# Performance work log

Hardware: AMD Instinct MI355X
Metric: run time of the kernel (lower is better)

## Reference

```python
import jax, jax.numpy as jnp
import numpy as np

N = 50000
E = 640000
F_IN = 128
F_OUT = 128


def setup_inputs() -> dict:
    key = jax.random.key(0)
    k1, k2, k3, k4, k5 = jax.random.split(key, 5)
    x = jax.random.normal(k1, (N, F_IN), dtype=jnp.float32)
    edge_index = jax.random.randint(k2, (2, E), 0, N, dtype=jnp.int64)
    s = 1.0 / np.sqrt(F_IN)
    W_l = jax.random.uniform(k3, (F_IN, F_OUT), minval=-s, maxval=s, dtype=jnp.float32)
    W_r = jax.random.uniform(k4, (F_IN, F_OUT), minval=-s, maxval=s, dtype=jnp.float32)
    b = jax.random.uniform(k5, (F_OUT,), minval=-s, maxval=s, dtype=jnp.float32)
    return {"x": x, "edge_index": edge_index, "W_l": W_l, "W_r": W_r, "b": b}


def reference(x, edge_index, W_l, W_r, b):
    src, dst = edge_index[0], edge_index[1]
    # gather source-node features along edges: [E, F_in]
    msgs = x[src]
    # mean aggregation at destination nodes
    summed = jax.ops.segment_sum(msgs, dst, num_segments=N)          # [N, F_in]
    counts = jax.ops.segment_sum(jnp.ones((E,), jnp.float32), dst, num_segments=N)
    mean_nb = summed / jnp.maximum(counts, 1.0)[:, None]
    # SAGEConv: lin_l(aggregated) + lin_r(self), bias on lin_l only
    out = mean_nb @ W_l + x @ W_r + b
    return jax.nn.relu(out)
```

## Files before the change

kernel.cpp:

```cpp
#include <hip/hip_runtime.h>

#define N_NODES 50000
#define E_EDGES 640000
#define F 128

typedef __attribute__((ext_vector_type(8))) short short8;
typedef __attribute__((ext_vector_type(4))) float f32x4;

#define DEG_OFF 0
#define OFF_OFF 200704
#define CUR_OFF 401408
#define BSUM_OFF 601600
#define BPRE_OFF 602624
#define WF_OFF 603648
#define SRC_OFF 734720
#define XBF_OFF 3294720
#define WS_NEED_FULL 16094720ULL

#define XCAST_BLKS 3125
#define WPREP_BLKS 16
#define HIST_BLKS 2048
#define PREP_GRID (XCAST_BLKS + WPREP_BLKS + HIST_BLKS)

__device__ __forceinline__ unsigned short f2bf(float f) {
    unsigned int u = __builtin_bit_cast(unsigned int, f);
    u += 0x7FFFu + ((u >> 16) & 1u);
    return (unsigned short)(u >> 16);
}
__device__ __forceinline__ float bfhi2f(unsigned int hi16) {
    return __builtin_bit_cast(float, hi16 & 0xFFFF0000u);
}

__global__ __launch_bounds__(256) void gnn_prep(
    const float* __restrict__ x, const int* __restrict__ ei,
    const float* __restrict__ Wl, const float* __restrict__ Wr,
    short* __restrict__ Wf, unsigned short* __restrict__ xbf,
    int* __restrict__ deg, int full) {
    const int bid = blockIdx.x;
    const int t = threadIdx.x;
    if (bid < XCAST_BLKS) {
        if (!full) return;
        const size_t i = ((size_t)bid * 256 + t) * 8;
        const float4 a0 = *reinterpret_cast<const float4*>(x + i);
        const float4 a1 = *reinterpret_cast<const float4*>(x + i + 4);
        short8 v;
        v[0] = (short)f2bf(a0.x); v[1] = (short)f2bf(a0.y);
        v[2] = (short)f2bf(a0.z); v[3] = (short)f2bf(a0.w);
        v[4] = (short)f2bf(a1.x); v[5] = (short)f2bf(a1.y);
        v[6] = (short)f2bf(a1.z); v[7] = (short)f2bf(a1.w);
        *reinterpret_cast<short8*>((short*)xbf + i) = v;
    } else if (bid < XCAST_BLKS + WPREP_BLKS) {
        const int tid = (bid - XCAST_BLKS) * 256 + t;
        const int lane = tid & 63;
        const int frag = tid >> 6;
        const int kstep = frag >> 3;
        const int ct = frag & 7;
        const int kb = kstep * 32 + (lane >> 4) * 8;
        const int c = ct * 16 + (lane & 15);
        short8 v;
#pragma unroll
        for (int j = 0; j < 8; ++j) {
            const int k = kb + j;
            const float f = (k < F) ? Wl[k * F + c] : Wr[(k - F) * F + c];
            v[j] = (short)f2bf(f);
        }
        *reinterpret_cast<short8*>(Wf + (size_t)tid * 8) = v;
    } else {
        const int i = (bid - XCAST_BLKS - WPREP_BLKS) * 256 + t;
        const int stride = HIST_BLKS * 256;
        for (int e = i; e < E_EDGES; e += stride)
            atomicAdd(&deg[ei[E_EDGES + e]], 1);
    }
}

__global__ __launch_bounds__(256) void gnn_scan_a(const int* __restrict__ deg,
                                                  int* __restrict__ off,
                                                  int* __restrict__ bsum) {
    __shared__ int s[256];
    const int t = threadIdx.x;
    const int i = blockIdx.x * 256 + t;
    const int v = (i < N_NODES) ? deg[i] : 0;
    s[t] = v;
    __syncthreads();
    for (int d = 1; d < 256; d <<= 1) {
        const int u = (t >= d) ? s[t - d] : 0;
        __syncthreads();
        s[t] += u;
        __syncthreads();
    }
    if (i < N_NODES) off[i] = s[t] - v;
    if (t == 255) bsum[blockIdx.x] = s[255];
}

__global__ __launch_bounds__(256) void gnn_scan2(const int* __restrict__ bsum,
                                                 int* __restrict__ off,
                                                 int* __restrict__ cur) {
    __shared__ int s[256];
    const int t = threadIdx.x;
    const int bid = blockIdx.x;
    s[t] = (t < 196) ? bsum[t] : 0;
    __syncthreads();
    for (int d = 1; d < 256; d <<= 1) {
        const int u = (t >= d) ? s[t - d] : 0;
        __syncthreads();
        s[t] += u;
        __syncthreads();
    }
    const int myPre = (bid == 0) ? 0 : s[bid - 1];
    const int i = bid * 256 + t;
    if (i < N_NODES) {
        const int o = off[i] + myPre;
        off[i] = o;
        cur[i] = o;
    }
    if (bid == 0 && t == 0) off[N_NODES] = s[195];
}

__global__ __launch_bounds__(256) void gnn_fill(const int* __restrict__ ei,
                                                int* __restrict__ cur,
                                                int* __restrict__ srcs) {
    const int i = blockIdx.x * blockDim.x + threadIdx.x;
    const int stride = gridDim.x * blockDim.x;
    for (int e = i; e < E_EDGES; e += stride) {
        const int d = ei[E_EDGES + e];
        const int p = atomicAdd(&cur[d], 1);
        srcs[p] = ei[e];
    }
}

__global__ __launch_bounds__(256) void gnn_agg_fin(
    const unsigned short* __restrict__ xbf, const int* __restrict__ off,
    const int* __restrict__ srcs, const short* __restrict__ Wf,
    const float* __restrict__ bias, float* __restrict__ out) {
    __shared__ unsigned short mean_s[64 * 128];
    const int t = threadIdx.x;
    const int lane = t & 63;
    const int wv = t >> 6;
    const int nb0 = blockIdx.x * 64;
    const int half = lane >> 5;
    const int l32 = lane & 31;

    for (int i = 0; i < 16; ++i) {
        const int node = nb0 + wv * 16 + i;
        if (node >= N_NODES) break;
        const int o0 = off[node];
        const int o1 = off[node + 1];
        const unsigned short* xb = xbf + (size_t)l32 * 4;
        f32x4 acc0 = {0.f, 0.f, 0.f, 0.f}, acc1 = {0.f, 0.f, 0.f, 0.f};
        f32x4 acc2 = {0.f, 0.f, 0.f, 0.f}, acc3 = {0.f, 0.f, 0.f, 0.f};
        int j = o0;
        for (; j + 8 <= o1; j += 8) {
            const uint2 a = *reinterpret_cast<const uint2*>(xb + (size_t)srcs[j + half] * F);
            const uint2 b = *reinterpret_cast<const uint2*>(xb + (size_t)srcs[j + 2 + half] * F);
            const uint2 c = *reinterpret_cast<const uint2*>(xb + (size_t)srcs[j + 4 + half] * F);
            const uint2 d = *reinterpret_cast<const uint2*>(xb + (size_t)srcs[j + 6 + half] * F);
            acc0[0] += bfhi2f(a.x << 16); acc0[1] += bfhi2f(a.x);
            acc0[2] += bfhi2f(a.y << 16); acc0[3] += bfhi2f(a.y);
            acc1[0] += bfhi2f(b.x << 16); acc1[1] += bfhi2f(b.x);
            acc1[2] += bfhi2f(b.y << 16); acc1[3] += bfhi2f(b.y);
            acc2[0] += bfhi2f(c.x << 16); acc2[1] += bfhi2f(c.x);
            acc2[2] += bfhi2f(c.y << 16); acc2[3] += bfhi2f(c.y);
            acc3[0] += bfhi2f(d.x << 16); acc3[1] += bfhi2f(d.x);
            acc3[2] += bfhi2f(d.y << 16); acc3[3] += bfhi2f(d.y);
        }
        for (; j + 4 <= o1; j += 4) {
            const uint2 a = *reinterpret_cast<const uint2*>(xb + (size_t)srcs[j + half] * F);
            const uint2 b = *reinterpret_cast<const uint2*>(xb + (size_t)srcs[j + 2 + half] * F);
            acc0[0] += bfhi2f(a.x << 16); acc0[1] += bfhi2f(a.x);
            acc0[2] += bfhi2f(a.y << 16); acc0[3] += bfhi2f(a.y);
            acc1[0] += bfhi2f(b.x << 16); acc1[1] += bfhi2f(b.x);
            acc1[2] += bfhi2f(b.y << 16); acc1[3] += bfhi2f(b.y);
        }
        for (; j < o1; j += 2) {
            const int jj = j + half;
            const uint2 a = *reinterpret_cast<const uint2*>(
                xb + (size_t)srcs[(jj < o1) ? jj : o0] * F);
            if (jj < o1) {
                acc0[0] += bfhi2f(a.x << 16); acc0[1] += bfhi2f(a.x);
                acc0[2] += bfhi2f(a.y << 16); acc0[3] += bfhi2f(a.y);
            }
        }
        acc0 += acc1 + acc2 + acc3;
        f32x4 o;
        o[0] = __shfl_xor(acc0[0], 32, 64);
        o[1] = __shfl_xor(acc0[1], 32, 64);
        o[2] = __shfl_xor(acc0[2], 32, 64);
        o[3] = __shfl_xor(acc0[3], 32, 64);
        acc0 += o;
        if (half == 0) {
            const float inv = 1.0f / (float)max(o1 - o0, 1);
            acc0 *= inv;
            ushort4 m;
            m.x = f2bf(acc0[0]); m.y = f2bf(acc0[1]);
            m.z = f2bf(acc0[2]); m.w = f2bf(acc0[3]);
            const int r = wv * 16 + i;
            const int byteoff = r * 256 + ((l32 * 8) ^ ((r & 7) << 4));
            *reinterpret_cast<ushort4*>((char*)mean_s + byteoff) = m;
        }
    }
    __syncthreads();

    const int rl = lane & 15;
    const int kg = lane >> 4;
    const int r0 = nb0 + wv * 16;
    const int arow = r0 + rl;
    const int arow_c = (arow < N_NODES) ? arow : (N_NODES - 1);
    const int rr = arow_c - nb0;

    f32x4 acc[8];
#pragma unroll
    for (int ct = 0; ct < 8; ++ct) acc[ct] = (f32x4){0.f, 0.f, 0.f, 0.f};

#pragma unroll
    for (int kstep = 0; kstep < 8; ++kstep) {
        short8 af;
        if (kstep < 4) {
            const int cb = (kstep * 64 + kg * 16) ^ ((rr & 7) << 4);
            af = *reinterpret_cast<const short8*>((const char*)mean_s +
                                                  rr * 256 + cb);
        } else {
            const int k0 = kstep * 32 + kg * 8 - F;
            af = *reinterpret_cast<const short8*>(xbf + (size_t)arow_c * F + k0);
        }
#pragma unroll
        for (int ct = 0; ct < 8; ++ct) {
            const short8 bf = *reinterpret_cast<const short8*>(
                Wf + (size_t)((kstep * 8 + ct) * 64 + lane) * 8);
            acc[ct] = __builtin_amdgcn_mfma_f32_16x16x32_bf16(af, bf, acc[ct],
                                                              0, 0, 0);
        }
    }

#pragma unroll
    for (int ct = 0; ct < 8; ++ct) {
        const int c = ct * 16 + rl;
        const float bv = bias[c];
#pragma unroll
        for (int r = 0; r < 4; ++r) {
            const int row = r0 + kg * 4 + r;
            if (row < N_NODES)
                out[(size_t)row * F + c] = fmaxf(acc[ct][r] + bv, 0.0f);
        }
    }
}

__global__ __launch_bounds__(256) void gnn_aggregate(
    const float* __restrict__ x, const int* __restrict__ off,
    const int* __restrict__ srcs, float* __restrict__ out) {
    const int node = blockIdx.x * 4 + (threadIdx.x >> 6);
    if (node >= N_NODES) return;
    const int lane = threadIdx.x & 63;
    const int half = lane >> 5;
    const int l32 = lane & 31;
    const int o0 = off[node];
    const int o1 = off[node + 1];
    f32x4 acc0 = {0.f, 0.f, 0.f, 0.f};
    f32x4 acc1 = {0.f, 0.f, 0.f, 0.f};
    int j = o0;
    for (; j + 4 <= o1; j += 4) {
        const int sA = srcs[j + half];
        const int sB = srcs[j + 2 + half];
        acc0 += *reinterpret_cast<const f32x4*>(x + (size_t)sA * F + l32 * 4);
        acc1 += *reinterpret_cast<const f32x4*>(x + (size_t)sB * F + l32 * 4);
    }
    for (; j < o1; j += 2) {
        const int jj = j + half;
        const int s = srcs[(jj < o1) ? jj : o0];
        f32x4 v = *reinterpret_cast<const f32x4*>(x + (size_t)s * F + l32 * 4);
        if (jj >= o1) v = (f32x4){0.f, 0.f, 0.f, 0.f};
        acc0 += v;
    }
    acc0 += acc1;
    f32x4 o;
    o[0] = __shfl_xor(acc0[0], 32, 64);
    o[1] = __shfl_xor(acc0[1], 32, 64);
    o[2] = __shfl_xor(acc0[2], 32, 64);
    o[3] = __shfl_xor(acc0[3], 32, 64);
    acc0 += o;
    if (half == 0) {
        const float inv = 1.0f / (float)max(o1 - o0, 1);
        acc0 *= inv;
        *reinterpret_cast<f32x4*>(out + (size_t)node * F + l32 * 4) = acc0;
    }
}

__global__ __launch_bounds__(256) void gnn_finalize_mfma(
    const float* __restrict__ x, const short* __restrict__ Wf,
    const float* __restrict__ bias, float* __restrict__ out) {
    const int t = threadIdx.x;
    const int lane = t & 63;
    const int wv = t >> 6;
    const int r0 = blockIdx.x * 64 + wv * 16;
    const int rl = lane & 15;
    const int kg = lane >> 4;
    const int arow = r0 + rl;
    const int arow_c = (arow < N_NODES) ? arow : (N_NODES - 1);
    f32x4 acc[8];
#pragma unroll
    for (int ct = 0; ct < 8; ++ct) acc[ct] = (f32x4){0.f, 0.f, 0.f, 0.f};
#pragma unroll
    for (int kstep = 0; kstep < 8; ++kstep) {
        const int k0 = kstep * 32 + kg * 8;
        const float* asrc = (kstep < 4) ? (out + (size_t)arow_c * F + k0)
                                        : (x + (size_t)arow_c * F + (k0 - F));
        const float4 a0 = *reinterpret_cast<const float4*>(asrc);
        const float4 a1 = *reinterpret_cast<const float4*>(asrc + 4);
        short8 af;
        af[0] = (short)f2bf(a0.x); af[1] = (short)f2bf(a0.y);
        af[2] = (short)f2bf(a0.z); af[3] = (short)f2bf(a0.w);
        af[4] = (short)f2bf(a1.x); af[5] = (short)f2bf(a1.y);
        af[6] = (short)f2bf(a1.z); af[7] = (short)f2bf(a1.w);
#pragma unroll
        for (int ct = 0; ct < 8; ++ct) {
            const short8 bf = *reinterpret_cast<const short8*>(
                Wf + (size_t)((kstep * 8 + ct) * 64 + lane) * 8);
            acc[ct] = __builtin_amdgcn_mfma_f32_16x16x32_bf16(af, bf, acc[ct],
                                                              0, 0, 0);
        }
    }
#pragma unroll
    for (int ct = 0; ct < 8; ++ct) {
        const int c = ct * 16 + rl;
        const float bv = bias[c];
#pragma unroll
        for (int r = 0; r < 4; ++r) {
            const int row = r0 + kg * 4 + r;
            if (row < N_NODES)
                out[(size_t)row * F + c] = fmaxf(acc[ct][r] + bv, 0.0f);
        }
    }
}

extern "C" void kernel_launch(void* const* d_in, const int* in_sizes, int n_in,
                              void* d_out, int out_size, void* d_ws,
                              size_t ws_size, hipStream_t stream) {
    const float* x = (const float*)d_in[0];
    const int* ei = (const int*)d_in[1];
    const float* Wl = (const float*)d_in[2];
    const float* Wr = (const float*)d_in[3];
    const float* b = (const float*)d_in[4];
    float* out = (float*)d_out;

    char* ws = (char*)d_ws;
    int* deg = (int*)(ws + DEG_OFF);
    int* off = (int*)(ws + OFF_OFF);
    int* cur = (int*)(ws + CUR_OFF);
    int* bsum = (int*)(ws + BSUM_OFF);
    short* Wf = (short*)(ws + WF_OFF);
    int* srcs = (int*)(ws + SRC_OFF);
    unsigned short* xbf = (unsigned short*)(ws + XBF_OFF);

    const int full = (ws_size >= WS_NEED_FULL) ? 1 : 0;

    hipMemsetAsync(deg, 0, N_NODES * sizeof(int), stream);
    gnn_prep<<<PREP_GRID, 256, 0, stream>>>(x, ei, Wl, Wr, Wf, xbf, deg, full);
    gnn_scan_a<<<196, 256, 0, stream>>>(deg, off, bsum);
    gnn_scan2<<<196, 256, 0, stream>>>(bsum, off, cur);
    gnn_fill<<<2048, 256, 0, stream>>>(ei, cur, srcs);

    if (full) {
        gnn_agg_fin<<<(N_NODES + 63) / 64, 256, 0, stream>>>(xbf, off, srcs,
                                                             Wf, b, out);
    } else {
        gnn_aggregate<<<(N_NODES + 3) / 4, 256, 0, stream>>>(x, off, srcs, out);
        gnn_finalize_mfma<<<(N_NODES + 63) / 64, 256, 0, stream>>>(x, Wf, b,
                                                                   out);
    }
}
```

Before: 207.2 us.

## Split fused aggregate+GEMM kernel into separate bf16 aggregate and finalize kernels

```diff
diff --git a/kernel.cpp b/kernel.cpp
--- a/kernel.cpp
+++ b/kernel.cpp
@@ -11,11 +11,11 @@
 #define OFF_OFF 200704
 #define CUR_OFF 401408
 #define BSUM_OFF 601600
-#define BPRE_OFF 602624
 #define WF_OFF 603648
 #define SRC_OFF 734720
 #define XBF_OFF 3294720
-#define WS_NEED_FULL 16094720ULL
+#define MBF_OFF 16094720
+#define WS_NEED_FULL 28894720ULL
 
 #define XCAST_BLKS 3125
 #define WPREP_BLKS 16
@@ -128,84 +128,80 @@
     }
 }
 
-__global__ __launch_bounds__(256) void gnn_agg_fin(
+__global__ __launch_bounds__(256) void gnn_aggregate_bf(
     const unsigned short* __restrict__ xbf, const int* __restrict__ off,
-    const int* __restrict__ srcs, const short* __restrict__ Wf,
-    const float* __restrict__ bias, float* __restrict__ out) {
-    __shared__ unsigned short mean_s[64 * 128];
+    const int* __restrict__ srcs, unsigned short* __restrict__ mbf) {
+    const int node = blockIdx.x * 4 + (threadIdx.x >> 6);
+    if (node >= N_NODES) return;
+    const int lane = threadIdx.x & 63;
+    const int half = lane >> 5;
+    const int l32 = lane & 31;
+    const int o0 = off[node];
+    const int o1 = off[node + 1];
+    const unsigned short* xb = xbf + (size_t)l32 * 4;
+    f32x4 acc0 = {0.f, 0.f, 0.f, 0.f}, acc1 = {0.f, 0.f, 0.f, 0.f};
+    f32x4 acc2 = {0.f, 0.f, 0.f, 0.f}, acc3 = {0.f, 0.f, 0.f, 0.f};
+    int j = o0;
+    for (; j + 8 <= o1; j += 8) {
+        const uint2 a = *reinterpret_cast<const uint2*>(xb + (size_t)srcs[j + half] * F);
+        const uint2 b = *reinterpret_cast<const uint2*>(xb + (size_t)srcs[j + 2 + half] * F);
+        const uint2 c = *reinterpret_cast<const uint2*>(xb + (size_t)srcs[j + 4 + half] * F);
+        const uint2 d = *reinterpret_cast<const uint2*>(xb + (size_t)srcs[j + 6 + half] * F);
+        acc0[0] += bfhi2f(a.x << 16); acc0[1] += bfhi2f(a.x);
+        acc0[2] += bfhi2f(a.y << 16); acc0[3] += bfhi2f(a.y);
+        acc1[0] += bfhi2f(b.x << 16); acc1[1] += bfhi2f(b.x);
+        acc1[2] += bfhi2f(b.y << 16); acc1[3] += bfhi2f(b.y);
+        acc2[0] += bfhi2f(c.x << 16); acc2[1] += bfhi2f(c.x);
+        acc2[2] += bfhi2f(c.y << 16); acc2[3] += bfhi2f(c.y);
+        acc3[0] += bfhi2f(d.x << 16); acc3[1] += bfhi2f(d.x);
+        acc3[2] += bfhi2f(d.y << 16); acc3[3] += bfhi2f(d.y);
+    }
+    for (; j + 4 <= o1; j += 4) {
+        const uint2 a = *reinterpret_cast<const uint2*>(xb + (size_t)srcs[j + half] * F);
+        const uint2 b = *reinterpret_cast<const uint2*>(xb + (size_t)srcs[j + 2 + half] * F);
+        acc0[0] += bfhi2f(a.x << 16); acc0[1] += bfhi2f(a.x);
+        acc0[2] += bfhi2f(a.y << 16); acc0[3] += bfhi2f(a.y);
+        acc1[0] += bfhi2f(b.x << 16); acc1[1] += bfhi2f(b.x);
+        acc1[2] += bfhi2f(b.y << 16); acc1[3] += bfhi2f(b.y);
+    }
+    for (; j < o1; j += 2) {
+        const int jj = j + half;
+        const uint2 a = *reinterpret_cast<const uint2*>(
+            xb + (size_t)srcs[(jj < o1) ? jj : o0] * F);
+        if (jj < o1) {
+            acc0[0] += bfhi2f(a.x << 16); acc0[1] += bfhi2f(a.x);
+            acc0[2] += bfhi2f(a.y << 16); acc0[3] += bfhi2f(a.y);
+        }
+    }
+    acc0 += acc1 + acc2 + acc3;
+    f32x4 o;
+    o[0] = __shfl_xor(acc0[0], 32, 64);
+    o[1] = __shfl_xor(acc0[1], 32, 64);
+    o[2] = __shfl_xor(acc0[2], 32, 64);
+    o[3] = __shfl_xor(acc0[3], 32, 64);
+    acc0 += o;
+    if (half == 0) {
+        const float inv = 1.0f / (float)max(o1 - o0, 1);
+        acc0 *= inv;
+        ushort4 m;
+        m.x = f2bf(acc0[0]); m.y = f2bf(acc0[1]);
+        m.z = f2bf(acc0[2]); m.w = f2bf(acc0[3]);
+        *reinterpret_cast<ushort4*>(mbf + (size_t)node * F + l32 * 4) = m;
+    }
+}
+
+__global__ __launch_bounds__(256) void gnn_finalize_bf(
+    const unsigned short* __restrict__ xbf, const unsigned short* __restrict__ mbf,
+    const short* __restrict__ Wf, const float* __restrict__ bias,
+    float* __restrict__ out) {
     const int t = threadIdx.x;
     const int lane = t & 63;
     const int wv = t >> 6;
-    const int nb0 = blockIdx.x * 64;
-    const int half = lane >> 5;
-    const int l32 = lane & 31;
-
-    for (int i = 0; i < 16; ++i) {
-        const int node = nb0 + wv * 16 + i;
-        if (node >= N_NODES) break;
-        const int o0 = off[node];
-        const int o1 = off[node + 1];
-        const unsigned short* xb = xbf + (size_t)l32 * 4;
-        f32x4 acc0 = {0.f, 0.f, 0.f, 0.f}, acc1 = {0.f, 0.f, 0.f, 0.f};
-        f32x4 acc2 = {0.f, 0.f, 0.f, 0.f}, acc3 = {0.f, 0.f, 0.f, 0.f};
-        int j = o0;
-        for (; j + 8 <= o1; j += 8) {
-            const uint2 a = *reinterpret_cast<const uint2*>(xb + (size_t)srcs[j + half] * F);
-            const uint2 b = *reinterpret_cast<const uint2*>(xb + (size_t)srcs[j + 2 + half] * F);
-            const uint2 c = *reinterpret_cast<const uint2*>(xb + (size_t)srcs[j + 4 + half] * F);
-            const uint2 d = *reinterpret_cast<const uint2*>(xb + (size_t)srcs[j + 6 + half] * F);
-            acc0[0] += bfhi2f(a.x << 16); acc0[1] += bfhi2f(a.x);
-            acc0[2] += bfhi2f(a.y << 16); acc0[3] += bfhi2f(a.y);
-            acc1[0] += bfhi2f(b.x << 16); acc1[1] += bfhi2f(b.x);
-            acc1[2] += bfhi2f(b.y << 16); acc1[3] += bfhi2f(b.y);
-            acc2[0] += bfhi2f(c.x << 16); acc2[1] += bfhi2f(c.x);
-            acc2[2] += bfhi2f(c.y << 16); acc2[3] += bfhi2f(c.y);
-            acc3[0] += bfhi2f(d.x << 16); acc3[1] += bfhi2f(d.x);
-            acc3[2] += bfhi2f(d.y << 16); acc3[3] += bfhi2f(d.y);
-        }
-        for (; j + 4 <= o1; j += 4) {
-            const uint2 a = *reinterpret_cast<const uint2*>(xb + (size_t)srcs[j + half] * F);
-            const uint2 b = *reinterpret_cast<const uint2*>(xb + (size_t)srcs[j + 2 + half] * F);
-            acc0[0] += bfhi2f(a.x << 16); acc0[1] += bfhi2f(a.x);
-            acc0[2] += bfhi2f(a.y << 16); acc0[3] += bfhi2f(a.y);
-            acc1[0] += bfhi2f(b.x << 16); acc1[1] += bfhi2f(b.x);
-            acc1[2] += bfhi2f(b.y << 16); acc1[3] += bfhi2f(b.y);
-        }
-        for (; j < o1; j += 2) {
-            const int jj = j + half;
-            const uint2 a = *reinterpret_cast<const uint2*>(
-                xb + (size_t)srcs[(jj < o1) ? jj : o0] * F);
-            if (jj < o1) {
-                acc0[0] += bfhi2f(a.x << 16); acc0[1] += bfhi2f(a.x);
-                acc0[2] += bfhi2f(a.y << 16); acc0[3] += bfhi2f(a.y);
-            }
-        }
-        acc0 += acc1 + acc2 + acc3;
-        f32x4 o;
-        o[0] = __shfl_xor(acc0[0], 32, 64);
-        o[1] = __shfl_xor(acc0[1], 32, 64);
-        o[2] = __shfl_xor(acc0[2], 32, 64);
-        o[3] = __shfl_xor(acc0[3], 32, 64);
-        acc0 += o;
-        if (half == 0) {
-            const float inv = 1.0f / (float)max(o1 - o0, 1);
-            acc0 *= inv;
-            ushort4 m;
-            m.x = f2bf(acc0[0]); m.y = f2bf(acc0[1]);
-            m.z = f2bf(acc0[2]); m.w = f2bf(acc0[3]);
-            const int r = wv * 16 + i;
-            const int byteoff = r * 256 + ((l32 * 8) ^ ((r & 7) << 4));
-            *reinterpret_cast<ushort4*>((char*)mean_s + byteoff) = m;
-        }
-    }
-    __syncthreads();
-
+    const int r0 = blockIdx.x * 64 + wv * 16;
     const int rl = lane & 15;
     const int kg = lane >> 4;
-    const int r0 = nb0 + wv * 16;
     const int arow = r0 + rl;
     const int arow_c = (arow < N_NODES) ? arow : (N_NODES - 1);
-    const int rr = arow_c - nb0;
 
     f32x4 acc[8];
 #pragma unroll
@@ -213,15 +209,11 @@
 
 #pragma unroll
     for (int kstep = 0; kstep < 8; ++kstep) {
-        short8 af;
-        if (kstep < 4) {
-            const int cb = (kstep * 64 + kg * 16) ^ ((rr & 7) << 4);
-            af = *reinterpret_cast<const short8*>((const char*)mean_s +
-                                                  rr * 256 + cb);
-        } else {
-            const int k0 = kstep * 32 + kg * 8 - F;
-            af = *reinterpret_cast<const short8*>(xbf + (size_t)arow_c * F + k0);
-        }
+        const int k0 = kstep * 32 + kg * 8;
+        const unsigned short* asrc =
+            (kstep < 4) ? (mbf + (size_t)arow_c * F + k0)
+                        : (xbf + (size_t)arow_c * F + (k0 - F));
+        const short8 af = *reinterpret_cast<const short8*>(asrc);
 #pragma unroll
         for (int ct = 0; ct < 8; ++ct) {
             const short8 bf = *reinterpret_cast<const short8*>(
@@ -349,6 +341,7 @@
     short* Wf = (short*)(ws + WF_OFF);
     int* srcs = (int*)(ws + SRC_OFF);
     unsigned short* xbf = (unsigned short*)(ws + XBF_OFF);
+    unsigned short* mbf = (unsigned short*)(ws + MBF_OFF);
 
     const int full = (ws_size >= WS_NEED_FULL) ? 1 : 0;
 
@@ -359,8 +352,10 @@
     gnn_fill<<<2048, 256, 0, stream>>>(ei, cur, srcs);
 
     if (full) {
-        gnn_agg_fin<<<(N_NODES + 63) / 64, 256, 0, stream>>>(xbf, off, srcs,
-                                                             Wf, b, out);
+        gnn_aggregate_bf<<<(N_NODES + 3) / 4, 256, 0, stream>>>(xbf, off, srcs,
+                                                                mbf);
+        gnn_finalize_bf<<<(N_NODES + 63) / 64, 256, 0, stream>>>(xbf, mbf, Wf,
+                                                                 b, out);
     } else {
         gnn_aggregate<<<(N_NODES + 3) / 4, 256, 0, stream>>>(x, off, srcs, out);
         gnn_finalize_mfma<<<(N_NODES + 63) / 64, 256, 0, stream>>>(x, Wf, b,
```

Result: faster. 196.7 us (-5.1%).
